# Kernel tuning notes

Hardware: AMD Instinct MI355X
Metric: run time of the kernel (lower is better)

The kernel has to match this reference:

```python
import jax, jax.numpy as jnp
import numpy as np

RES = 192      # resolution
RANK = 8       # low-rank
FD = 32        # feature_dim
NFPD = 32      # num_features_per_dim = round(32768**(1/3))
RADIUS = 1.3
NI = 128       # n_intersections
STEP = 0.0352  # step_size
B = 2048       # rays


def setup_inputs():
    key = jax.random.key(0)
    ks = jax.random.split(key, 12)
    ro = jax.random.normal(ks[0], (B, 3), dtype=jnp.float32)
    ro = ro / jnp.linalg.norm(ro, axis=-1, keepdims=True) * 2.5  # origins outside the cube
    rd = -ro + 0.1 * jax.random.normal(ks[1], (B, 3), dtype=jnp.float32)
    rd = rd / jnp.linalg.norm(rd, axis=-1, keepdims=True)        # roughly toward origin
    def nrm(k, shape, std):
        return std * jax.random.normal(k, shape, dtype=jnp.float32)
    return {
        "rays_o": ro, "rays_d": rd,
        "Gxy": nrm(ks[2], (RES, RES, 3, RANK), 0.1),
        "Gxz": nrm(ks[3], (RES, RES, 3, RANK), 0.1),
        "Gyz": nrm(ks[4], (RES, RES, 3, RANK), 0.1),
        "F_grid": nrm(ks[5], (NFPD, NFPD, NFPD, FD), 0.05),
        "sW0": nrm(ks[6], (FD, 128), FD ** -0.5),
        "sW1": nrm(ks[7], (128, 128), 128 ** -0.5),
        "sW2": nrm(ks[8], (128, 16), 128 ** -0.5),
        "cW0": nrm(ks[9], (31, 64), 31 ** -0.5),
        "cW1": nrm(ks[10], (64, 64), 64 ** -0.5),
        "cW2": nrm(ks[11], (64, 3), 64 ** -0.5),
    }


def trilinear(vol, coords):
    # vol: [D,H,W,C]; coords: [N,3] as (x,y,z) in [-1,1]; x indexes W (last spatial dim)
    # matches torch grid_sample(align_corners=True, mode='bilinear', padding_mode='border')
    D, H, W, C = vol.shape
    def prep(c, size):
        idx = jnp.clip((c + 1.0) * 0.5 * (size - 1), 0.0, size - 1.0)  # border clamp
        i0 = jnp.clip(jnp.floor(idx).astype(jnp.int32), 0, size - 2)
        return i0, i0 + 1, idx - i0
    x0, x1, wx = prep(coords[:, 0], W)
    y0, y1, wy = prep(coords[:, 1], H)
    z0, z1, wz = prep(coords[:, 2], D)
    wx = wx[:, None]; wy = wy[:, None]; wz = wz[:, None]
    def g(zi, yi, xi):
        return vol[zi, yi, xi]  # [N,C]
    c00 = g(z0, y0, x0) * (1 - wx) + g(z0, y0, x1) * wx
    c01 = g(z0, y1, x0) * (1 - wx) + g(z0, y1, x1) * wx
    c10 = g(z1, y0, x0) * (1 - wx) + g(z1, y0, x1) * wx
    c11 = g(z1, y1, x0) * (1 - wx) + g(z1, y1, x1) * wx
    c0 = c00 * (1 - wy) + c01 * wy
    c1 = c10 * (1 - wy) + c11 * wy
    return c0 * (1 - wz) + c1 * wz


def sh16(d):
    # tcnn SphericalHarmonics degree 4 on directions (input (d+1)/2 is unmapped back to d internally)
    x, y, z = d[:, 0], d[:, 1], d[:, 2]
    x2, y2, z2 = x * x, y * y, z * z
    return jnp.stack([
        jnp.full_like(x, 0.28209479177387814),
        -0.48860251190291987 * y,
        0.48860251190291987 * z,
        -0.48860251190291987 * x,
        1.0925484305920792 * x * y,
        -1.0925484305920792 * y * z,
        0.94617469575755997 * z2 - 0.31539156525251999,
        -1.0925484305920792 * x * z,
        0.54627421529603959 * (x2 - y2),
        0.59004358992664352 * y * (-3.0 * x2 + y2),
        2.8906114426405538 * x * y * z,
        0.45704579946446572 * y * (1.0 - 5.0 * z2),
        0.3731763325901154 * z * (5.0 * z2 - 3.0),
        0.45704579946446572 * x * (1.0 - 5.0 * z2),
        1.445305721320277 * z * (x2 - y2),
        0.59004358992664352 * x * (-x2 + 3.0 * y2),
    ], axis=-1)


def _forward(rays_o, rays_d, Gxy, Gxz, Gyz, F_grid, sW0, sW1, sW2, cW0, cW1, cW2):
    b = rays_o.shape[0]
    # --- get_intersections: ray/AABB [-R,R]^3, uniform marching ---
    d = jnp.where(jnp.abs(rays_d) < 1e-9, 1e-9, rays_d)
    t1 = (-RADIUS - rays_o) / d
    t2 = (RADIUS - rays_o) / d
    tmin = jnp.max(jnp.minimum(t1, t2), axis=-1)
    tmax = jnp.min(jnp.maximum(t1, t2), axis=-1)
    near = jnp.maximum(tmin, 0.0)
    ts = near[:, None] + jnp.arange(NI + 1, dtype=jnp.float32) * STEP  # intersections [B,NI+1]
    tmid = 0.5 * (ts[:, :-1] + ts[:, 1:])                              # [B,NI]
    pts = rays_o[:, None, :] + tmid[..., None] * rays_d[:, None, :]    # [B,NI,3]
    mask = (jnp.all(jnp.abs(pts) <= RADIUS, axis=-1)
            & (tmid <= tmax[:, None]) & (tmax > tmin)[:, None])        # [B,NI]
    rdn = rays_d / jnp.linalg.norm(rays_d, axis=-1, keepdims=True)
    # coordinate chain of forward + eval_pts nets out to pts/RADIUS in [-1,1]
    p = ((pts / RADIUS + 1.0) * RES / 2.0) * 2.0 / RES - 1.0
    pf = p.reshape(-1, 3)
    # --- densify low-rank tri-plane grid: sum_r Gxy*Gxz*Gyz -> [RES,RES,RES,3] ---
    grid = jnp.zeros((RES, RES, RES, 3), dtype=Gxy.dtype)
    for r in range(RANK):  # fixed small rank; avoids a [RES^3,3,RANK] intermediate
        grid = grid + (Gxy[:, :, None, :, r] * Gxz[:, None, :, :, r] * Gyz[None, :, :, :, r])
    # --- eval_pts: grid_sample -> hash-feature grid_sample -> MLPs ---
    Gvals = trilinear(grid, pf)            # [N,3]
    Fvals = trilinear(F_grid, Gvals)       # [N,FD]
    h = jax.nn.relu(Fvals @ sW0)
    h = jax.nn.relu(h @ sW1)
    out16 = h @ sW2                        # [N,16]
    sigma = out16[:, 0].reshape(b, NI)
    sigma = jax.nn.relu(jnp.where(mask, sigma, 0.0))
    rdn_pts = jnp.broadcast_to(rdn[:, None, :], (b, NI, 3)).reshape(-1, 3)
    ci = jnp.concatenate([sh16(rdn_pts), out16[:, 1:]], axis=-1)  # [N,31]
    c = jax.nn.relu(ci @ cW0)
    c = jax.nn.relu(c @ cW1)
    color = (c @ cW2).reshape(b, NI, 3)
    color = jnp.where(mask[..., None], color, 0.0)
    # --- sigma2alpha + shrgb2rgb (white background) ---
    dists = ts[:, 1:] - ts[:, :-1]         # |rdn| == 1
    alpha = 1.0 - jnp.exp(-sigma * dists)
    T = jnp.cumprod(1.0 - alpha + 1e-10, axis=-1)
    T = jnp.concatenate([jnp.ones_like(T[:, :1]), T[:, :-1]], axis=-1)  # exclusive
    w = alpha * T                          # abs_light [B,NI]
    rgb = jax.nn.sigmoid(color)
    acc = jnp.sum(w, axis=-1)
    return jnp.sum(w[..., None] * rgb, axis=1) + (1.0 - acc)[..., None]  # [B,3]


def reference(rays_o, rays_d, Gxy, Gxz, Gyz, F_grid, sW0, sW1, sW2, cW0, cW1, cW2):
    return _forward(rays_o, rays_d, Gxy, Gxz, Gyz, F_grid, sW0, sW1, sW2, cW0, cW1, cW2)
```

## Files before the change

### kernel.cpp

```cpp
#include <hip/hip_runtime.h>
#include <math.h>

#define RES 192
#define RANK 8
#define NI 128
#define LW 132

typedef __attribute__((ext_vector_type(8))) _Float16 h8;
typedef __attribute__((ext_vector_type(4))) _Float16 h4;
typedef __attribute__((ext_vector_type(2))) _Float16 h2f;
typedef __attribute__((ext_vector_type(4))) float floatx4;

#define OFF_SW0 0
#define OFF_SW1 4096
#define OFF_SW2 20480
#define OFF_CW0 22528
#define OFF_CW1 24576
#define OFF_CW2 28672
#define PACK_TOTAL 29696

#define TRI_CELLS (RES*RES)
#define CELLS3    (3*TRI_CELLS)
#define FG_TOTAL  (32*32*32*32)
#define PREP2_TOTAL (PACK_TOTAL + CELLS3 + FG_TOTAL/8)

__device__ __forceinline__ void prep_idx(float c, int size, int& i0, float& f){
    float idx = (c + 1.0f)*0.5f*(float)(size-1);
    idx = fminf(fmaxf(idx, 0.0f), (float)(size-1));
    int ii = (int)idx;
    if (ii > size-2) ii = size-2;
    i0 = ii;
    f = idx - (float)ii;
}

__device__ __forceinline__ float wred64(float v){
    #pragma unroll
    for (int o=32;o>0;o>>=1) v += __shfl_down(v, o, 64);
    return v;
}

__device__ __forceinline__ h8 shx1(h8 v){
    union { h8 h; int i[4]; } u; u.h = v;
    #pragma unroll
    for (int k=0;k<4;k++) u.i[k] = __shfl_xor(u.i[k], 1, 64);
    return u.h;
}

__device__ __forceinline__ h8 ld8(const _Float16* p){
    h4 lo = *(const h4*)p;
    h4 hi = *(const h4*)(p+4);
    return __builtin_shufflevector(lo, hi, 0,1,2,3,4,5,6,7);
}
__device__ __forceinline__ void st8(_Float16* p, h8 v){
    *(h4*)p     = __builtin_shufflevector(v,v,0,1,2,3);
    *(h4*)(p+4) = __builtin_shufflevector(v,v,4,5,6,7);
}
__device__ __forceinline__ void st4r(_Float16* p, floatx4 v){
    h4 o = {(_Float16)fmaxf(v[0],0.f), (_Float16)fmaxf(v[1],0.f),
            (_Float16)fmaxf(v[2],0.f), (_Float16)fmaxf(v[3],0.f)};
    *(h4*)p = o;
}
__device__ __forceinline__ void st4n(_Float16* p, floatx4 v){
    h4 o = {(_Float16)v[0], (_Float16)v[1], (_Float16)v[2], (_Float16)v[3]};
    *(h4*)p = o;
}

__global__ void __launch_bounds__(256) prep_all2(
    const float* __restrict__ sW0, const float* __restrict__ sW1,
    const float* __restrict__ sW2, const float* __restrict__ cW0,
    const float* __restrict__ cW1, const float* __restrict__ cW2,
    const float* __restrict__ Gxy, const float* __restrict__ Gxz,
    const float* __restrict__ Gyz, const float* __restrict__ F_grid,
    _Float16* __restrict__ Wp, _Float16* __restrict__ Gp, _Float16* __restrict__ Fg)
{
    int e = blockIdx.x*256 + threadIdx.x;
    if (e < PACK_TOTAL){
        const float* src; int K, N, ksteps, base;
        bool cw0remap = false;
        if      (e < OFF_SW1){ src=sW0; K=32;  N=128; ksteps=1; base=OFF_SW0; }
        else if (e < OFF_SW2){ src=sW1; K=128; N=128; ksteps=4; base=OFF_SW1; }
        else if (e < OFF_CW0){ src=sW2; K=128; N=16;  ksteps=4; base=OFF_SW2; }
        else if (e < OFF_CW1){ src=cW0; K=31;  N=64;  ksteps=1; base=OFF_CW0; cw0remap=true; }
        else if (e < OFF_CW2){ src=cW1; K=64;  N=64;  ksteps=2; base=OFF_CW1; }
        else                 { src=cW2; K=64;  N=3;   ksteps=2; base=OFF_CW2; }
        int i = e - base;
        int j = i & 7, lane = (i>>3)&63, t = i>>9;
        int ks = t % ksteps, nt = t / ksteps;
        int k = ks*32 + (lane>>4)*8 + j;
        int n = nt*16 + (lane&15);
        float v;
        if (cw0remap){
            v = 0.0f;
            if (k != 16 && n < N){
                int ksrc = (k < 16) ? k : k-1;
                v = src[ksrc*N + n];
            }
        } else {
            v = (k < K && n < N) ? src[k*N + n] : 0.0f;
        }
        Wp[e] = (_Float16)v;
        return;
    }
    int e2 = e - PACK_TOTAL;
    if (e2 < CELLS3){
        int p, lc;
        if      (e2 < TRI_CELLS)   { p = 0; lc = e2; }
        else if (e2 < 2*TRI_CELLS) { p = 1; lc = e2 - TRI_CELLS; }
        else                       { p = 2; lc = e2 - 2*TRI_CELLS; }
        const float* src = ((p==0) ? Gxy : (p==1) ? Gxz : Gyz) + (size_t)lc*24;
        const float4* s4 = (const float4*)src;
        float4 a = s4[0], b = s4[1], c = s4[2], d = s4[3], ee = s4[4], ff = s4[5];
        h8 o0 = {(_Float16)a.x,(_Float16)a.y,(_Float16)a.z,(_Float16)a.w,
                 (_Float16)b.x,(_Float16)b.y,(_Float16)b.z,(_Float16)b.w};
        h8 o1 = {(_Float16)c.x,(_Float16)c.y,(_Float16)c.z,(_Float16)c.w,
                 (_Float16)d.x,(_Float16)d.y,(_Float16)d.z,(_Float16)d.w};
        h8 o2 = {(_Float16)ee.x,(_Float16)ee.y,(_Float16)ee.z,(_Float16)ee.w,
                 (_Float16)ff.x,(_Float16)ff.y,(_Float16)ff.z,(_Float16)ff.w};
        h8 zz = {0,0,0,0,0,0,0,0};
        h8* dst = (h8*)(Gp + (size_t)e2*32);
        dst[0]=o0; dst[1]=o1; dst[2]=o2; dst[3]=zz;
        return;
    }
    int t = e2 - CELLS3;
    const float4* s4 = (const float4*)(F_grid + (size_t)t*8);
    float4 a = s4[0], b = s4[1];
    h8 o = {(_Float16)a.x,(_Float16)a.y,(_Float16)a.z,(_Float16)a.w,
            (_Float16)b.x,(_Float16)b.y,(_Float16)b.z,(_Float16)b.w};
    ((h8*)Fg)[t] = o;
}

__launch_bounds__(256, 4)
__global__ void nerf_fused(
    const float* __restrict__ rays_o, const float* __restrict__ rays_d,
    const _Float16* __restrict__ Gp, const _Float16* __restrict__ Fg,
    const _Float16* __restrict__ Wp, float* __restrict__ out)
{
    __shared__ _Float16 buf[128*LW];
    __shared__ float sigmaArr[128];
    __shared__ float rgbArr[128*3];
    __shared__ float wtot[2];
    __shared__ float partial[8];

    const int tid  = threadIdx.x;
    const int lane = tid & 63;
    const int wv   = tid >> 6;
    const int ray  = blockIdx.x;

    const int rowbase = wv*32;
    const int col  = lane & 15;
    const int quad = lane >> 4;
    const int ar0  = rowbase + col;
    const int ar1  = ar0 + 16;

    const float ox = rays_o[ray*3+0], oy = rays_o[ray*3+1], oz = rays_o[ray*3+2];
    const float dx = rays_d[ray*3+0], dy = rays_d[ray*3+1], dz = rays_d[ray*3+2];

    float sdx = (fabsf(dx) < 1e-9f) ? 1e-9f : dx;
    float sdy = (fabsf(dy) < 1e-9f) ? 1e-9f : dy;
    float sdz = (fabsf(dz) < 1e-9f) ? 1e-9f : dz;
    float t1x = (-1.3f - ox)/sdx, t2x = (1.3f - ox)/sdx;
    float t1y = (-1.3f - oy)/sdy, t2y = (1.3f - oy)/sdy;
    float t1z = (-1.3f - oz)/sdz, t2z = (1.3f - oz)/sdz;
    float tmin = fmaxf(fminf(t1x,t2x), fmaxf(fminf(t1y,t2y), fminf(t1z,t2z)));
    float tmax = fminf(fmaxf(t1x,t2x), fminf(fmaxf(t1y,t2y), fmaxf(t1z,t2z)));
    float nearv = fmaxf(tmin, 0.0f);

    bool skipAll;
    {
        int sid = rowbase + (lane & 31);
        float w_ts0 = nearv + (float)sid     * 0.0352f;
        float w_ts1 = nearv + (float)(sid+1) * 0.0352f;
        float w_tm  = 0.5f*(w_ts0+w_ts1);
        float wpx = ox + w_tm*dx, wpy = oy + w_tm*dy, wpz = oz + w_tm*dz;
        bool m = (fabsf(wpx)<=1.3f) && (fabsf(wpy)<=1.3f) && (fabsf(wpz)<=1.3f)
               && (w_tm<=tmax) && (tmax>tmin);
        skipAll = (__ballot(m) == 0ULL);
    }

    if (!skipAll){
        {
            const int s = rowbase + (lane >> 1);
            const int h = lane & 1;

            float ts0 = nearv + (float)s     * 0.0352f;
            float ts1 = nearv + (float)(s+1) * 0.0352f;
            float tmid = 0.5f*(ts0+ts1);
            float px = ox + tmid*dx, py = oy + tmid*dy, pz = oz + tmid*dz;
            bool mask = (fabsf(px)<=1.3f) && (fabsf(py)<=1.3f) && (fabsf(pz)<=1.3f)
                      && (tmid<=tmax) && (tmax>tmin);

            h8 FVa = {0,0,0,0,0,0,0,0};
            h8 FVb = {0,0,0,0,0,0,0,0};

            if (mask){
                float p0 = (px/1.3f + 1.0f)*192.0f/2.0f*2.0f/192.0f - 1.0f;
                float p1 = (py/1.3f + 1.0f)*192.0f/2.0f*2.0f/192.0f - 1.0f;
                float p2 = (pz/1.3f + 1.0f)*192.0f/2.0f*2.0f/192.0f - 1.0f;

                int x0, y0, z0; float fx, fy, fz;
                prep_idx(p0, RES, x0, fx);
                prep_idx(p1, RES, y0, fy);
                prep_idx(p2, RES, z0, fz);

                const int zi  = z0 + h;
                const float wzc = h ? fz : (1.0f - fz);
                const int yiA = y0 + h;
                const int yiB = y0 + 1 - h;

                h8 XYA[3], XYB[3], XZ0[3], XZ1[3], YZo0[3], YZo1[3];
                {
                    const int oxyA = (zi*RES + yiA)*32;
                    const int oxyB = (zi*RES + yiB)*32;
                    const int ox0  = (TRI_CELLS + zi*RES + x0)*32;
                    const int oy0  = (2*TRI_CELLS + yiA*RES + x0)*32;
                    const h8* pxyA = (const h8*)(Gp + oxyA);
                    const h8* pxyB = (const h8*)(Gp + oxyB);
                    const h8* px0  = (const h8*)(Gp + ox0);
                    const h8* px1  = (const h8*)(Gp + ox0 + 32);
                    const h8* py0  = (const h8*)(Gp + oy0);
                    const h8* py1  = (const h8*)(Gp + oy0 + 32);
                    #pragma unroll
                    for (int q=0;q<3;q++){
                        XYA[q]=pxyA[q]; XYB[q]=pxyB[q];
                        XZ0[q]=px0[q];  XZ1[q]=px1[q];
                        YZo0[q]=py0[q]; YZo1[q]=py1[q];
                    }
                }
                h8 YZp0[3], YZp1[3];
                #pragma unroll
                for (int q=0;q<3;q++){ YZp0[q]=shx1(YZo0[q]); YZp1[q]=shx1(YZo1[q]); }

                const float wyA = h ? fy : (1.0f - fy);
                const float wyB = h ? (1.0f - fy) : fy;

                h8 ACC0 = {0,0,0,0,0,0,0,0};
                h8 ACC1 = {0,0,0,0,0,0,0,0};
                h8 ACC2 = {0,0,0,0,0,0,0,0};
                #pragma unroll
                for (int yo=0; yo<2; yo++){
                    const float wy = yo ? wyB : wyA;
                    #pragma unroll
                    for (int xc=0; xc<2; xc++){
                        const float wx = xc ? fx : (1.0f - fx);
                        const _Float16 wh = (_Float16)(wzc*wy*wx);
                        const h8 w8 = {wh,wh,wh,wh,wh,wh,wh,wh};
                        h8 Q0, Q1, Q2;
                        if (yo==0){
                            const h8* YZv = xc ? YZo1 : YZo0;
                            Q0 = (XYA[0]*(xc?XZ1[0]:XZ0[0]))*YZv[0];
                            Q1 = (XYA[1]*(xc?XZ1[1]:XZ0[1]))*YZv[1];
                            Q2 = (XYA[2]*(xc?XZ1[2]:XZ0[2]))*YZv[2];
                        } else {
                            const h8* YZv = xc ? YZp1 : YZp0;
                            Q0 = (XYB[0]*(xc?XZ1[0]:XZ0[0]))*YZv[0];
                            Q1 = (XYB[1]*(xc?XZ1[1]:XZ0[1]))*YZv[1];
                            Q2 = (XYB[2]*(xc?XZ1[2]:XZ0[2]))*YZv[2];
                        }
                        ACC0 = __builtin_elementwise_fma(Q0, w8, ACC0);
                        ACC1 = __builtin_elementwise_fma(Q1, w8, ACC1);
                        ACC2 = __builtin_elementwise_fma(Q2, w8, ACC2);
                    }
                }
                h2f a0h = __builtin_shufflevector(ACC0,ACC0,0,1) + __builtin_shufflevector(ACC0,ACC0,2,3);
                h2f b0h = __builtin_shufflevector(ACC0,ACC0,4,5) + __builtin_shufflevector(ACC0,ACC0,6,7);
                h2f c0h = a0h + b0h;
                float gv0 = (float)c0h[0] + (float)c0h[1];
                h2f a1h = __builtin_shufflevector(ACC1,ACC1,0,1) + __builtin_shufflevector(ACC1,ACC1,2,3);
                h2f b1h = __builtin_shufflevector(ACC1,ACC1,4,5) + __builtin_shufflevector(ACC1,ACC1,6,7);
                h2f c1h = a1h + b1h;
                float gv1 = (float)c1h[0] + (float)c1h[1];
                h2f a2h = __builtin_shufflevector(ACC2,ACC2,0,1) + __builtin_shufflevector(ACC2,ACC2,2,3);
                h2f b2h = __builtin_shufflevector(ACC2,ACC2,4,5) + __builtin_shufflevector(ACC2,ACC2,6,7);
                h2f c2h = a2h + b2h;
                float gv2 = (float)c2h[0] + (float)c2h[1];

                gv0 += __shfl_xor(gv0, 1, 64);
                gv1 += __shfl_xor(gv1, 1, 64);
                gv2 += __shfl_xor(gv2, 1, 64);

                int a0,b0,c0; float fa,fb,fc;
                prep_idx(gv2, 32, a0, fa);
                prep_idx(gv1, 32, b0, fb);
                prep_idx(gv0, 32, c0, fc);
                #pragma unroll
                for (int zc=0; zc<2; zc++){
                    const int zi2 = a0+zc; const float wz2 = zc ? fa : 1.f-fa;
                    #pragma unroll
                    for (int yc=0; yc<2; yc++){
                        const int yi2 = b0+yc; const float wy2 = yc ? fb : 1.f-fb;
                        #pragma unroll
                        for (int xc=0; xc<2; xc++){
                            const int xi2 = c0+xc; const float wx2 = xc ? fc : 1.f-fc;
                            const _Float16 wh = (_Float16)(wz2*wy2*wx2);
                            const h8 w8 = {wh,wh,wh,wh,wh,wh,wh,wh};
                            const int fo = ((zi2*32+yi2)*32+xi2)*32 + h*16;
                            const h8* pf = (const h8*)(Fg + fo);
                            FVa = __builtin_elementwise_fma(pf[0], w8, FVa);
                            FVb = __builtin_elementwise_fma(pf[1], w8, FVb);
                        }
                    }
                }
            }

            st8(&buf[s*LW + h*16],     FVa);
            st8(&buf[s*LW + h*16 + 8], FVb);
        }

        {
            h8 a0 = ld8(&buf[ar0*LW + quad*8]);
            h8 a1 = ld8(&buf[ar1*LW + quad*8]);
            const h8* W = (const h8*)(Wp + OFF_SW0);
            #pragma unroll
            for (int nt=0; nt<8; nt++){
                h8 b = W[nt*64 + lane];
                floatx4 c0v = {0.f,0.f,0.f,0.f}, c1v = {0.f,0.f,0.f,0.f};
                c0v = __builtin_amdgcn_mfma_f32_16x16x32_f16(b, a0, c0v, 0,0,0);
                c1v = __builtin_amdgcn_mfma_f32_16x16x32_f16(b, a1, c1v, 0,0,0);
                st4r(&buf[ar0*LW + nt*16 + quad*4], c0v);
                st4r(&buf[ar1*LW + nt*16 + quad*4], c1v);
            }
        }

        {
            h8 A0[4], A1[4];
            #pragma unroll
            for (int ks=0;ks<4;ks++){
                A0[ks] = ld8(&buf[ar0*LW + ks*32 + quad*8]);
                A1[ks] = ld8(&buf[ar1*LW + ks*32 + quad*8]);
            }
            const h8* W = (const h8*)(Wp + OFF_SW1);
            #pragma unroll
            for (int nt=0; nt<8; nt++){
                floatx4 c0v = {0.f,0.f,0.f,0.f}, c1v = {0.f,0.f,0.f,0.f};
                #pragma unroll
                for (int ks=0;ks<4;ks++){
                    h8 b = W[(nt*4+ks)*64 + lane];
                    c0v = __builtin_amdgcn_mfma_f32_16x16x32_f16(b, A0[ks], c0v, 0,0,0);
                    c1v = __builtin_amdgcn_mfma_f32_16x16x32_f16(b, A1[ks], c1v, 0,0,0);
                }
                st4r(&buf[ar0*LW + nt*16 + quad*4], c0v);
                st4r(&buf[ar1*LW + nt*16 + quad*4], c1v);
            }
        }

        {
            h8 A0[4], A1[4];
            #pragma unroll
            for (int ks=0;ks<4;ks++){
                A0[ks] = ld8(&buf[ar0*LW + ks*32 + quad*8]);
                A1[ks] = ld8(&buf[ar1*LW + ks*32 + quad*8]);
            }
            const h8* W = (const h8*)(Wp + OFF_SW2);
            floatx4 c0v = {0.f,0.f,0.f,0.f}, c1v = {0.f,0.f,0.f,0.f};
            #pragma unroll
            for (int ks=0;ks<4;ks++){
                h8 b = W[ks*64 + lane];
                c0v = __builtin_amdgcn_mfma_f32_16x16x32_f16(b, A0[ks], c0v, 0,0,0);
                c1v = __builtin_amdgcn_mfma_f32_16x16x32_f16(b, A1[ks], c1v, 0,0,0);
            }
            st4n(&buf[ar0*LW + 16 + quad*4], c0v);
            st4n(&buf[ar1*LW + 16 + quad*4], c1v);
            if (quad == 0){
                sigmaArr[ar0] = c0v[0];
                sigmaArr[ar1] = c1v[0];
            }
            const float dn = sqrtf(dx*dx+dy*dy+dz*dz);
            const float X = dx/dn, Y = dy/dn, Z = dz/dn;
            const float X2=X*X, Y2=Y*Y, Z2=Z*Z;
            float sh[16];
            sh[0]= 0.28209479177387814f;
            sh[1]=-0.48860251190291987f*Y;
            sh[2]= 0.48860251190291987f*Z;
            sh[3]=-0.48860251190291987f*X;
            sh[4]= 1.0925484305920792f*X*Y;
            sh[5]=-1.0925484305920792f*Y*Z;
            sh[6]= 0.94617469575756f*Z2 - 0.31539156525252f;
            sh[7]=-1.0925484305920792f*X*Z;
            sh[8]= 0.5462742152960396f*(X2-Y2);
            sh[9]= 0.5900435899266435f*Y*(-3.0f*X2+Y2);
            sh[10]=2.890611442640554f*X*Y*Z;
            sh[11]=0.4570457994644657f*Y*(1.0f-5.0f*Z2);
            sh[12]=0.3731763325901154f*Z*(5.0f*Z2-3.0f);
            sh[13]=0.4570457994644657f*X*(1.0f-5.0f*Z2);
            sh[14]=1.445305721320277f*Z*(X2-Y2);
            sh[15]=0.5900435899266435f*X*(-X2+3.0f*Y2);
            if (lane < 32){
                int row = rowbase + lane;
                #pragma unroll
                for (int jb=0;jb<4;jb++){
                    h4 o = {(_Float16)sh[jb*4+0], (_Float16)sh[jb*4+1],
                            (_Float16)sh[jb*4+2], (_Float16)sh[jb*4+3]};
                    *(h4*)&buf[row*LW + jb*4] = o;
                }
            }
        }

        {
            h8 a0 = ld8(&buf[ar0*LW + quad*8]);
            h8 a1 = ld8(&buf[ar1*LW + quad*8]);
            const h8* W = (const h8*)(Wp + OFF_CW0);
            #pragma unroll
            for (int nt=0; nt<4; nt++){
                h8 b = W[nt*64 + lane];
                floatx4 c0v = {0.f,0.f,0.f,0.f}, c1v = {0.f,0.f,0.f,0.f};
                c0v = __builtin_amdgcn_mfma_f32_16x16x32_f16(b, a0, c0v, 0,0,0);
                c1v = __builtin_amdgcn_mfma_f32_16x16x32_f16(b, a1, c1v, 0,0,0);
                st4r(&buf[ar0*LW + nt*16 + quad*4], c0v);
                st4r(&buf[ar1*LW + nt*16 + quad*4], c1v);
            }
        }

        {
            h8 A0[2], A1[2];
            #pragma unroll
            for (int ks=0;ks<2;ks++){
                A0[ks] = ld8(&buf[ar0*LW + ks*32 + quad*8]);
                A1[ks] = ld8(&buf[ar1*LW + ks*32 + quad*8]);
            }
            const h8* W = (const h8*)(Wp + OFF_CW1);
            #pragma unroll
            for (int nt=0; nt<4; nt++){
                floatx4 c0v = {0.f,0.f,0.f,0.f}, c1v = {0.f,0.f,0.f,0.f};
                #pragma unroll
                for (int ks=0;ks<2;ks++){
                    h8 b = W[(nt*2+ks)*64 + lane];
                    c0v = __builtin_amdgcn_mfma_f32_16x16x32_f16(b, A0[ks], c0v, 0,0,0);
                    c1v = __builtin_amdgcn_mfma_f32_16x16x32_f16(b, A1[ks], c1v, 0,0,0);
                }
                st4r(&buf[ar0*LW + nt*16 + quad*4], c0v);
                st4r(&buf[ar1*LW + nt*16 + quad*4], c1v);
            }
        }

        {
            h8 A0[2], A1[2];
            #pragma unroll
            for (int ks=0;ks<2;ks++){
                A0[ks] = ld8(&buf[ar0*LW + ks*32 + quad*8]);
                A1[ks] = ld8(&buf[ar1*LW + ks*32 + quad*8]);
            }
            const h8* W = (const h8*)(Wp + OFF_CW2);
            floatx4 c0v = {0.f,0.f,0.f,0.f}, c1v = {0.f,0.f,0.f,0.f};
            #pragma unroll
            for (int ks=0;ks<2;ks++){
                h8 b = W[ks*64 + lane];
                c0v = __builtin_amdgcn_mfma_f32_16x16x32_f16(b, A0[ks], c0v, 0,0,0);
                c1v = __builtin_amdgcn_mfma_f32_16x16x32_f16(b, A1[ks], c1v, 0,0,0);
            }
            if (quad == 0){
                rgbArr[ar0*3+0] = c0v[0];
                rgbArr[ar0*3+1] = c0v[1];
                rgbArr[ar0*3+2] = c0v[2];
                rgbArr[ar1*3+0] = c1v[0];
                rgbArr[ar1*3+1] = c1v[1];
                rgbArr[ar1*3+2] = c1v[2];
            }
        }
    }

    __syncthreads();

    {
        float alpha = 0.f, rr = 0.f, rg = 0.f, rb = 0.f;
        if (tid < 128){
            float ts0 = nearv + (float)tid     * 0.0352f;
            float ts1 = nearv + (float)(tid+1) * 0.0352f;
            float tmid = 0.5f*(ts0+ts1);
            float dist = ts1 - ts0;
            float px = ox + tmid*dx, py = oy + tmid*dy, pz = oz + tmid*dz;
            bool mask = (fabsf(px)<=1.3f) && (fabsf(py)<=1.3f) && (fabsf(pz)<=1.3f)
                      && (tmid<=tmax) && (tmax>tmin);
            float sg = mask ? fmaxf(sigmaArr[tid], 0.f) : 0.f;
            alpha = 1.0f - expf(-sg*dist);
            if (mask){
                rr = 1.0f/(1.0f+expf(-rgbArr[tid*3+0]));
                rg = 1.0f/(1.0f+expf(-rgbArr[tid*3+1]));
                rb = 1.0f/(1.0f+expf(-rgbArr[tid*3+2]));
            }
        }
        float p = 1.0f - alpha + 1e-10f;
        #pragma unroll
        for (int off=1; off<64; off<<=1){
            float u = __shfl_up(p, off, 64);
            if (lane >= off) p *= u;
        }
        if (tid < 128 && lane == 63) wtot[wv] = p;
        float excl = __shfl_up(p, 1, 64);
        if (lane == 0) excl = 1.0f;
        __syncthreads();
        if (tid < 128){
            float T = excl;
            if (wv == 1) T *= wtot[0];
            float w = alpha * T;
            float v0 = wred64(w*rr);
            float v1 = wred64(w*rg);
            float v2 = wred64(w*rb);
            float v3 = wred64(w);
            if (lane == 0){
                partial[wv*4+0]=v0; partial[wv*4+1]=v1; partial[wv*4+2]=v2; partial[wv*4+3]=v3;
            }
        }
        __syncthreads();
        if (tid == 0){
            float acc = partial[3] + partial[7];
            float bg  = 1.0f - acc;
            out[ray*3+0] = partial[0] + partial[4] + bg;
            out[ray*3+1] = partial[1] + partial[5] + bg;
            out[ray*3+2] = partial[2] + partial[6] + bg;
        }
    }
}

extern "C" void kernel_launch(void* const* d_in, const int* in_sizes, int n_in,
                              void* d_out, int out_size, void* d_ws, size_t ws_size,
                              hipStream_t stream){
    const float* rays_o = (const float*)d_in[0];
    const float* rays_d = (const float*)d_in[1];
    const float* Gxy    = (const float*)d_in[2];
    const float* Gxz    = (const float*)d_in[3];
    const float* Gyz    = (const float*)d_in[4];
    const float* F_grid = (const float*)d_in[5];
    const float* sW0    = (const float*)d_in[6];
    const float* sW1    = (const float*)d_in[7];
    const float* sW2    = (const float*)d_in[8];
    const float* cW0    = (const float*)d_in[9];
    const float* cW1    = (const float*)d_in[10];
    const float* cW2    = (const float*)d_in[11];

    _Float16* Wp = (_Float16*)d_ws;
    _Float16* Gp = Wp + PACK_TOTAL;
    _Float16* Fg = Gp + (size_t)3*TRI_CELLS*32;

    prep_all2<<<PREP2_TOTAL/256, 256, 0, stream>>>(sW0,sW1,sW2,cW0,cW1,cW2,
                                                   Gxy,Gxz,Gyz,F_grid, Wp,Gp,Fg);
    nerf_fused<<<2048, 256, 0, stream>>>(rays_o, rays_d, Gp, Fg, Wp, (float*)d_out);
}
```

Measured before the change: 131.0 us.

## Keep MLP activations in registers by permuting weight K-layout instead of LDS

Removes the 33 KB shared-memory activation buffer used between MLP layers. The packed weights are reordered along K so that each MFMA output fragment (4 halves per lane) can be concatenated directly into the next layer's A operand. Cross-lane shuffles handle the feature input and the SH/color-input assembly. This drops the LDS round trips, and the smaller LDS footprint allows the occupancy hint to rise from 4 to 5 blocks, at the cost of more live registers.

```diff
diff --git a/kernel.cpp b/kernel.cpp
--- a/kernel.cpp
+++ b/kernel.cpp
@@ -4,7 +4,6 @@
 #define RES 192
 #define RANK 8
 #define NI 128
-#define LW 132
 
 typedef __attribute__((ext_vector_type(8))) _Float16 h8;
 typedef __attribute__((ext_vector_type(4))) _Float16 h4;
@@ -45,24 +44,31 @@
     for (int k=0;k<4;k++) u.i[k] = __shfl_xor(u.i[k], 1, 64);
     return u.h;
 }
-
-__device__ __forceinline__ h8 ld8(const _Float16* p){
-    h4 lo = *(const h4*)p;
-    h4 hi = *(const h4*)(p+4);
+__device__ __forceinline__ h8 shfl8(h8 v, int src){
+    union { h8 h; int i[4]; } u; u.h = v;
+    #pragma unroll
+    for (int k=0;k<4;k++) u.i[k] = __shfl(u.i[k], src, 64);
+    return u.h;
+}
+__device__ __forceinline__ h4 shfl4(h4 v, int src){
+    union { h4 h; int i[2]; } u; u.h = v;
+    #pragma unroll
+    for (int k=0;k<2;k++) u.i[k] = __shfl(u.i[k], src, 64);
+    return u.h;
+}
+__device__ __forceinline__ h8 cat44(h4 lo, h4 hi){
     return __builtin_shufflevector(lo, hi, 0,1,2,3,4,5,6,7);
 }
-__device__ __forceinline__ void st8(_Float16* p, h8 v){
-    *(h4*)p     = __builtin_shufflevector(v,v,0,1,2,3);
-    *(h4*)(p+4) = __builtin_shufflevector(v,v,4,5,6,7);
-}
-__device__ __forceinline__ void st4r(_Float16* p, floatx4 v){
-    h4 o = {(_Float16)fmaxf(v[0],0.f), (_Float16)fmaxf(v[1],0.f),
-            (_Float16)fmaxf(v[2],0.f), (_Float16)fmaxf(v[3],0.f)};
-    *(h4*)p = o;
-}
-__device__ __forceinline__ void st4n(_Float16* p, floatx4 v){
-    h4 o = {(_Float16)v[0], (_Float16)v[1], (_Float16)v[2], (_Float16)v[3]};
-    *(h4*)p = o;
+__device__ __forceinline__ h4 pk4r(floatx4 v){
+    return h4{(_Float16)fmaxf(v[0],0.f), (_Float16)fmaxf(v[1],0.f),
+              (_Float16)fmaxf(v[2],0.f), (_Float16)fmaxf(v[3],0.f)};
+}
+__device__ __forceinline__ h4 pk4n(floatx4 v){
+    return h4{(_Float16)v[0], (_Float16)v[1], (_Float16)v[2], (_Float16)v[3]};
+}
+__device__ __forceinline__ h8 pack8f(const float* s){
+    return h8{(_Float16)s[0],(_Float16)s[1],(_Float16)s[2],(_Float16)s[3],
+              (_Float16)s[4],(_Float16)s[5],(_Float16)s[6],(_Float16)s[7]};
 }
 
 __global__ void __launch_bounds__(256) prep_all2(
@@ -75,29 +81,28 @@
 {
     int e = blockIdx.x*256 + threadIdx.x;
     if (e < PACK_TOTAL){
-        const float* src; int K, N, ksteps, base;
-        bool cw0remap = false;
-        if      (e < OFF_SW1){ src=sW0; K=32;  N=128; ksteps=1; base=OFF_SW0; }
-        else if (e < OFF_SW2){ src=sW1; K=128; N=128; ksteps=4; base=OFF_SW1; }
-        else if (e < OFF_CW0){ src=sW2; K=128; N=16;  ksteps=4; base=OFF_SW2; }
-        else if (e < OFF_CW1){ src=cW0; K=31;  N=64;  ksteps=1; base=OFF_CW0; cw0remap=true; }
-        else if (e < OFF_CW2){ src=cW1; K=64;  N=64;  ksteps=2; base=OFF_CW1; }
-        else                 { src=cW2; K=64;  N=3;   ksteps=2; base=OFF_CW2; }
+        const float* src; int K, N, ksteps, base, wt;
+        if      (e < OFF_SW1){ src=sW0; K=32;  N=128; ksteps=1; base=OFF_SW0; wt=0; }
+        else if (e < OFF_SW2){ src=sW1; K=128; N=128; ksteps=4; base=OFF_SW1; wt=1; }
+        else if (e < OFF_CW0){ src=sW2; K=128; N=16;  ksteps=4; base=OFF_SW2; wt=1; }
+        else if (e < OFF_CW1){ src=cW0; K=31;  N=64;  ksteps=1; base=OFF_CW0; wt=2; }
+        else if (e < OFF_CW2){ src=cW1; K=64;  N=64;  ksteps=2; base=OFF_CW1; wt=1; }
+        else                 { src=cW2; K=64;  N=3;   ksteps=2; base=OFF_CW2; wt=1; }
         int i = e - base;
         int j = i & 7, lane = (i>>3)&63, t = i>>9;
         int ks = t % ksteps, nt = t / ksteps;
-        int k = ks*32 + (lane>>4)*8 + j;
-        int n = nt*16 + (lane&15);
-        float v;
-        if (cw0remap){
-            v = 0.0f;
-            if (k != 16 && n < N){
-                int ksrc = (k < 16) ? k : k-1;
-                v = src[ksrc*N + n];
-            }
+        int q = lane>>4, cn = lane&15;
+        int n = nt*16 + cn;
+        int ksrc;
+        if (wt == 0){
+            ksrc = q*8 + j;
+        } else if (wt == 1){
+            ksrc = ks*32 + 16*(j>>2) + 4*q + (j&3);
         } else {
-            v = (k < K && n < N) ? src[k*N + n] : 0.0f;
-        }
+            if (q < 2) ksrc = 8*q + j;
+            else { int o = 8*(q&1) + j; ksrc = (o==0) ? -1 : 15+o; }
+        }
+        float v = (ksrc >= 0 && ksrc < K && n < N) ? src[ksrc*N + n] : 0.0f;
         Wp[e] = (_Float16)v;
         return;
     }
@@ -129,13 +134,12 @@
     ((h8*)Fg)[t] = o;
 }
 
-__launch_bounds__(256, 4)
+__launch_bounds__(256, 5)
 __global__ void nerf_fused(
     const float* __restrict__ rays_o, const float* __restrict__ rays_d,
     const _Float16* __restrict__ Gp, const _Float16* __restrict__ Fg,
     const _Float16* __restrict__ Wp, float* __restrict__ out)
 {
-    __shared__ _Float16 buf[128*LW];
     __shared__ float sigmaArr[128];
     __shared__ float rgbArr[128*3];
     __shared__ float wtot[2];
@@ -149,8 +153,6 @@
     const int rowbase = wv*32;
     const int col  = lane & 15;
     const int quad = lane >> 4;
-    const int ar0  = rowbase + col;
-    const int ar1  = ar0 + 16;
 
     const float ox = rays_o[ray*3+0], oy = rays_o[ray*3+1], oz = rays_o[ray*3+2];
     const float dx = rays_d[ray*3+0], dy = rays_d[ray*3+1], dz = rays_d[ray*3+2];
@@ -178,6 +180,8 @@
     }
 
     if (!skipAll){
+        h8 FVa = {0,0,0,0,0,0,0,0};
+        h8 FVb = {0,0,0,0,0,0,0,0};
         {
             const int s = rowbase + (lane >> 1);
             const int h = lane & 1;
@@ -188,9 +192,6 @@
             float px = ox + tmid*dx, py = oy + tmid*dy, pz = oz + tmid*dz;
             bool mask = (fabsf(px)<=1.3f) && (fabsf(py)<=1.3f) && (fabsf(pz)<=1.3f)
                       && (tmid<=tmax) && (tmax>tmin);
-
-            h8 FVa = {0,0,0,0,0,0,0,0};
-            h8 FVb = {0,0,0,0,0,0,0,0};
 
             if (mask){
                 float p0 = (px/1.3f + 1.0f)*192.0f/2.0f*2.0f/192.0f - 1.0f;
@@ -220,15 +221,15 @@
                     const h8* py0  = (const h8*)(Gp + oy0);
                     const h8* py1  = (const h8*)(Gp + oy0 + 32);
                     #pragma unroll
-                    for (int q=0;q<3;q++){
-                        XYA[q]=pxyA[q]; XYB[q]=pxyB[q];
-                        XZ0[q]=px0[q];  XZ1[q]=px1[q];
-                        YZo0[q]=py0[q]; YZo1[q]=py1[q];
+                    for (int q2=0;q2<3;q2++){
+                        XYA[q2]=pxyA[q2]; XYB[q2]=pxyB[q2];
+                        XZ0[q2]=px0[q2];  XZ1[q2]=px1[q2];
+                        YZo0[q2]=py0[q2]; YZo1[q2]=py1[q2];
                     }
                 }
                 h8 YZp0[3], YZp1[3];
                 #pragma unroll
-                for (int q=0;q<3;q++){ YZp0[q]=shx1(YZo0[q]); YZp1[q]=shx1(YZo1[q]); }
+                for (int q2=0;q2<3;q2++){ YZp0[q2]=shx1(YZo0[q2]); YZp1[q2]=shx1(YZo1[q2]); }
 
                 const float wyA = h ? fy : (1.0f - fy);
                 const float wyB = h ? (1.0f - fy) : fy;
@@ -301,69 +302,68 @@
                     }
                 }
             }
-
-            st8(&buf[s*LW + h*16],     FVa);
-            st8(&buf[s*LW + h*16 + 8], FVb);
-        }
-
-        {
-            h8 a0 = ld8(&buf[ar0*LW + quad*8]);
-            h8 a1 = ld8(&buf[ar1*LW + quad*8]);
+        }
+
+        h8 A1f[2];
+        #pragma unroll
+        for (int m=0; m<2; m++){
+            int srcl = 32*m + 2*col + (quad>>1);
+            h8 va = shfl8(FVa, srcl);
+            h8 vb = shfl8(FVb, srcl);
+            A1f[m] = (quad & 1) ? vb : va;
+        }
+
+        h4 pk1[2][8];
+        {
             const h8* W = (const h8*)(Wp + OFF_SW0);
             #pragma unroll
             for (int nt=0; nt<8; nt++){
                 h8 b = W[nt*64 + lane];
                 floatx4 c0v = {0.f,0.f,0.f,0.f}, c1v = {0.f,0.f,0.f,0.f};
-                c0v = __builtin_amdgcn_mfma_f32_16x16x32_f16(b, a0, c0v, 0,0,0);
-                c1v = __builtin_amdgcn_mfma_f32_16x16x32_f16(b, a1, c1v, 0,0,0);
-                st4r(&buf[ar0*LW + nt*16 + quad*4], c0v);
-                st4r(&buf[ar1*LW + nt*16 + quad*4], c1v);
-            }
-        }
-
-        {
-            h8 A0[4], A1[4];
-            #pragma unroll
-            for (int ks=0;ks<4;ks++){
-                A0[ks] = ld8(&buf[ar0*LW + ks*32 + quad*8]);
-                A1[ks] = ld8(&buf[ar1*LW + ks*32 + quad*8]);
-            }
+                c0v = __builtin_amdgcn_mfma_f32_16x16x32_f16(b, A1f[0], c0v, 0,0,0);
+                c1v = __builtin_amdgcn_mfma_f32_16x16x32_f16(b, A1f[1], c1v, 0,0,0);
+                pk1[0][nt] = pk4r(c0v);
+                pk1[1][nt] = pk4r(c1v);
+            }
+        }
+
+        h4 pk2[2][8];
+        {
             const h8* W = (const h8*)(Wp + OFF_SW1);
             #pragma unroll
             for (int nt=0; nt<8; nt++){
                 floatx4 c0v = {0.f,0.f,0.f,0.f}, c1v = {0.f,0.f,0.f,0.f};
                 #pragma unroll
-                for (int ks=0;ks<4;ks++){
-                    h8 b = W[(nt*4+ks)*64 + lane];
-                    c0v = __builtin_amdgcn_mfma_f32_16x16x32_f16(b, A0[ks], c0v, 0,0,0);
-                    c1v = __builtin_amdgcn_mfma_f32_16x16x32_f16(b, A1[ks], c1v, 0,0,0);
+                for (int ks=0; ks<4; ks++){
+                    h8 b  = W[(nt*4+ks)*64 + lane];
+                    h8 a0 = cat44(pk1[0][2*ks], pk1[0][2*ks+1]);
+                    h8 a1 = cat44(pk1[1][2*ks], pk1[1][2*ks+1]);
+                    c0v = __builtin_amdgcn_mfma_f32_16x16x32_f16(b, a0, c0v, 0,0,0);
+                    c1v = __builtin_amdgcn_mfma_f32_16x16x32_f16(b, a1, c1v, 0,0,0);
                 }
-                st4r(&buf[ar0*LW + nt*16 + quad*4], c0v);
-                st4r(&buf[ar1*LW + nt*16 + quad*4], c1v);
-            }
-        }
-
-        {
-            h8 A0[4], A1[4];
+                pk2[0][nt] = pk4r(c0v);
+                pk2[1][nt] = pk4r(c1v);
+            }
+        }
+
+        h8 AC1[2];
+        {
+            const h8* W = (const h8*)(Wp + OFF_SW2);
+            floatx4 d0 = {0.f,0.f,0.f,0.f}, d1 = {0.f,0.f,0.f,0.f};
             #pragma unroll
-            for (int ks=0;ks<4;ks++){
-                A0[ks] = ld8(&buf[ar0*LW + ks*32 + quad*8]);
-                A1[ks] = ld8(&buf[ar1*LW + ks*32 + quad*8]);
-            }
-            const h8* W = (const h8*)(Wp + OFF_SW2);
-            floatx4 c0v = {0.f,0.f,0.f,0.f}, c1v = {0.f,0.f,0.f,0.f};
-            #pragma unroll
-            for (int ks=0;ks<4;ks++){
-                h8 b = W[ks*64 + lane];
-                c0v = __builtin_amdgcn_mfma_f32_16x16x32_f16(b, A0[ks], c0v, 0,0,0);
-                c1v = __builtin_amdgcn_mfma_f32_16x16x32_f16(b, A1[ks], c1v, 0,0,0);
-            }
-            st4n(&buf[ar0*LW + 16 + quad*4], c0v);
-            st4n(&buf[ar1*LW + 16 + quad*4], c1v);
+            for (int ks=0; ks<4; ks++){
+                h8 b  = W[ks*64 + lane];
+                h8 a0 = cat44(pk2[0][2*ks], pk2[0][2*ks+1]);
+                h8 a1 = cat44(pk2[1][2*ks], pk2[1][2*ks+1]);
+                d0 = __builtin_amdgcn_mfma_f32_16x16x32_f16(b, a0, d0, 0,0,0);
+                d1 = __builtin_amdgcn_mfma_f32_16x16x32_f16(b, a1, d1, 0,0,0);
+            }
             if (quad == 0){
-                sigmaArr[ar0] = c0v[0];
-                sigmaArr[ar1] = c1v[0];
-            }
+                sigmaArr[rowbase + col]      = d0[0];
+                sigmaArr[rowbase + 16 + col] = d1[0];
+            }
+            h4 pk3_0 = pk4n(d0), pk3_1 = pk4n(d1);
+
             const float dn = sqrtf(dx*dx+dy*dy+dz*dz);
             const float X = dx/dn, Y = dy/dn, Z = dz/dn;
             const float X2=X*X, Y2=Y*Y, Z2=Z*Z;
@@ -384,76 +384,67 @@
             sh[13]=0.4570457994644657f*X*(1.0f-5.0f*Z2);
             sh[14]=1.445305721320277f*Z*(X2-Y2);
             sh[15]=0.5900435899266435f*X*(-X2+3.0f*Y2);
-            if (lane < 32){
-                int row = rowbase + lane;
-                #pragma unroll
-                for (int jb=0;jb<4;jb++){
-                    h4 o = {(_Float16)sh[jb*4+0], (_Float16)sh[jb*4+1],
-                            (_Float16)sh[jb*4+2], (_Float16)sh[jb*4+3]};
-                    *(h4*)&buf[row*LW + jb*4] = o;
-                }
-            }
-        }
-
-        {
-            h8 a0 = ld8(&buf[ar0*LW + quad*8]);
-            h8 a1 = ld8(&buf[ar1*LW + quad*8]);
+            h8 shlo = pack8f(sh);
+            h8 shhi = pack8f(sh+8);
+            h8 Ash  = (quad & 1) ? shhi : shlo;
+
+            int ilo = (quad & 1)*32 + col;
+            h4 lo0 = shfl4(pk3_0, ilo), hi0 = shfl4(pk3_0, ilo+16);
+            h4 lo1 = shfl4(pk3_1, ilo), hi1 = shfl4(pk3_1, ilo+16);
+            AC1[0] = (quad < 2) ? Ash : cat44(lo0, hi0);
+            AC1[1] = (quad < 2) ? Ash : cat44(lo1, hi1);
+        }
+
+        h4 pkc1[2][4];
+        {
             const h8* W = (const h8*)(Wp + OFF_CW0);
             #pragma unroll
             for (int nt=0; nt<4; nt++){
                 h8 b = W[nt*64 + lane];
                 floatx4 c0v = {0.f,0.f,0.f,0.f}, c1v = {0.f,0.f,0.f,0.f};
-                c0v = __builtin_amdgcn_mfma_f32_16x16x32_f16(b, a0, c0v, 0,0,0);
-                c1v = __builtin_amdgcn_mfma_f32_16x16x32_f16(b, a1, c1v, 0,0,0);
-                st4r(&buf[ar0*LW + nt*16 + quad*4], c0v);
-                st4r(&buf[ar1*LW + nt*16 + quad*4], c1v);
-            }
-        }
-
-        {
-            h8 A0[2], A1[2];
-            #pragma unroll
-            for (int ks=0;ks<2;ks++){
-                A0[ks] = ld8(&buf[ar0*LW + ks*32 + quad*8]);
-                A1[ks] = ld8(&buf[ar1*LW + ks*32 + quad*8]);
-            }
+                c0v = __builtin_amdgcn_mfma_f32_16x16x32_f16(b, AC1[0], c0v, 0,0,0);
+                c1v = __builtin_amdgcn_mfma_f32_16x16x32_f16(b, AC1[1], c1v, 0,0,0);
+                pkc1[0][nt] = pk4r(c0v);
+                pkc1[1][nt] = pk4r(c1v);
+            }
+        }
+
+        h4 pkc2[2][4];
+        {
             const h8* W = (const h8*)(Wp + OFF_CW1);
             #pragma unroll
             for (int nt=0; nt<4; nt++){
                 floatx4 c0v = {0.f,0.f,0.f,0.f}, c1v = {0.f,0.f,0.f,0.f};
                 #pragma unroll
-                for (int ks=0;ks<2;ks++){
-                    h8 b = W[(nt*2+ks)*64 + lane];
-                    c0v = __builtin_amdgcn_mfma_f32_16x16x32_f16(b, A0[ks], c0v, 0,0,0);
-                    c1v = __builtin_amdgcn_mfma_f32_16x16x32_f16(b, A1[ks], c1v, 0,0,0);
+                for (int ks=0; ks<2; ks++){
+                    h8 b  = W[(nt*2+ks)*64 + lane];
+                    h8 a0 = cat44(pkc1[0][2*ks], pkc1[0][2*ks+1]);
+                    h8 a1 = cat44(pkc1[1][2*ks], pkc1[1][2*ks+1]);
+                    c0v = __builtin_amdgcn_mfma_f32_16x16x32_f16(b, a0, c0v, 0,0,0);
+                    c1v = __builtin_amdgcn_mfma_f32_16x16x32_f16(b, a1, c1v, 0,0,0);
                 }
-                st4r(&buf[ar0*LW + nt*16 + quad*4], c0v);
-                st4r(&buf[ar1*LW + nt*16 + quad*4], c1v);
-            }
-        }
-
-        {
-            h8 A0[2], A1[2];
+                pkc2[0][nt] = pk4r(c0v);
+                pkc2[1][nt] = pk4r(c1v);
+            }
+        }
+
+        {
+            const h8* W = (const h8*)(Wp + OFF_CW2);
+            floatx4 d0 = {0.f,0.f,0.f,0.f}, d1 = {0.f,0.f,0.f,0.f};
             #pragma unroll
-            for (int ks=0;ks<2;ks++){
-                A0[ks] = ld8(&buf[ar0*LW + ks*32 + quad*8]);
-                A1[ks] = ld8(&buf[ar1*LW + ks*32 + quad*8]);
-            }
-            const h8* W = (const h8*)(Wp + OFF_CW2);
-            floatx4 c0v = {0.f,0.f,0.f,0.f}, c1v = {0.f,0.f,0.f,0.f};
-            #pragma unroll
-            for (int ks=0;ks<2;ks++){
-                h8 b = W[ks*64 + lane];
-                c0v = __builtin_amdgcn_mfma_f32_16x16x32_f16(b, A0[ks], c0v, 0,0,0);
-                c1v = __builtin_amdgcn_mfma_f32_16x16x32_f16(b, A1[ks], c1v, 0,0,0);
+            for (int ks=0; ks<2; ks++){
+                h8 b  = W[ks*64 + lane];
+                h8 a0 = cat44(pkc2[0][2*ks], pkc2[0][2*ks+1]);
+                h8 a1 = cat44(pkc2[1][2*ks], pkc2[1][2*ks+1]);
+                d0 = __builtin_amdgcn_mfma_f32_16x16x32_f16(b, a0, d0, 0,0,0);
+                d1 = __builtin_amdgcn_mfma_f32_16x16x32_f16(b, a1, d1, 0,0,0);
             }
             if (quad == 0){
-                rgbArr[ar0*3+0] = c0v[0];
-                rgbArr[ar0*3+1] = c0v[1];
-                rgbArr[ar0*3+2] = c0v[2];
-                rgbArr[ar1*3+0] = c1v[0];
-                rgbArr[ar1*3+1] = c1v[1];
-                rgbArr[ar1*3+2] = c1v[2];
+                #pragma unroll
+                for (int r=0;r<3;r++){
+                    rgbArr[(rowbase + col)*3 + r]      = d0[r];
+                    rgbArr[(rowbase + 16 + col)*3 + r] = d1[r];
+                }
             }
         }
     }
```

After: 157.5 us. 1.2x slower.
